# Kernel optimization log

Measured on AMD Instinct MI355X. Metric: run time of the kernel, lower is better.

Reference implementation:

```python
import jax, jax.numpy as jnp
import numpy as np

B, N, D = 16, 2048, 64

def setup_inputs() -> dict:
    key = jax.random.key(0)
    kq, kk, kv = jax.random.split(key, 3)
    q = jax.random.normal(kq, (B, N, D), dtype=jnp.float32)
    k = jax.random.normal(kk, (B, N, D), dtype=jnp.float32)
    v = jax.random.normal(kv, (B, N, D), dtype=jnp.float32)
    return {"q": q, "k": k, "v": v}

def reference(q, k, v):
    d_k = q.shape[-1]
    # scores: [B, N, N] = q @ k^T, scaled by 1/sqrt(d_k) (applied after matmul, as in source)
    scores = jnp.einsum('bnd,bmd->bnm', q, k)
    attn = jax.nn.softmax(scores / np.sqrt(d_k).astype(q.dtype), axis=-1)
    out = jnp.einsum('bnm,bmd->bnd', attn, v)
    return out
```

## Files before the change

kernel.cpp:

```cpp
#include <hip/hip_runtime.h>

#define B_  16
#define N_  2048
#define D_  64
#define QB  128
#define KB  64
#define NW  8

typedef __attribute__((ext_vector_type(8))) short short8;
typedef __attribute__((ext_vector_type(4))) float f32x4;

static __device__ __forceinline__ unsigned cvt_pk_bf16(float lo, float hi) {
  unsigned r;
  asm("v_cvt_pk_bf16_f32 %0, %1, %2" : "=v"(r) : "v"(lo), "v"(hi));
  return r;
}

union U8 { unsigned u[4]; short8 s8; };

__global__ __launch_bounds__(512, 2) void attn_fwd_kernel(
    const float* __restrict__ qg, const float* __restrict__ kg,
    const float* __restrict__ vg, float* __restrict__ outg) {
  __shared__ __align__(16) unsigned short Kl[KB * D_];
  __shared__ __align__(16) unsigned short Vt[D_ * KB];
  __shared__ __align__(16) unsigned short Pl[NW][16 * KB];

  const int tid = threadIdx.x;
  const int w  = tid >> 6;
  const int l  = tid & 63;
  const int g  = l >> 4;
  const int qi = l & 15;
  const int bidx = blockIdx.x;
  const int b  = bidx >> 4;
  const int qt = bidx & 15;
  const int q0 = qt * QB + w * 16;

  short8 qf[2];
  {
    const float* qp = qg + ((size_t)(b * N_ + q0 + qi)) * D_;
    const float s = 0.125f;
#pragma unroll
    for (int dc = 0; dc < 2; ++dc) {
      float4 f0 = *(const float4*)(qp + dc * 32 + g * 8);
      float4 f1 = *(const float4*)(qp + dc * 32 + g * 8 + 4);
      U8 u;
      u.u[0] = cvt_pk_bf16(f0.x * s, f0.y * s);
      u.u[1] = cvt_pk_bf16(f0.z * s, f0.w * s);
      u.u[2] = cvt_pk_bf16(f1.x * s, f1.y * s);
      u.u[3] = cvt_pk_bf16(f1.z * s, f1.w * s);
      qf[dc] = u.s8;
    }
  }

  f32x4 acc[4] = {{0,0,0,0},{0,0,0,0},{0,0,0,0},{0,0,0,0}};
  float m_run = -INFINITY;
  float l_run = 0.f;

  const float* kbase = kg + (size_t)b * N_ * D_;
  const float* vbase = vg + (size_t)b * N_ * D_;

  for (int kv0 = 0; kv0 < N_; kv0 += KB) {
#pragma unroll
    for (int p = 0; p < 2; ++p) {
      int idx = tid + p * 512;
      int row = idx >> 4, c4 = idx & 15;
      float4 f = *(const float4*)(kbase + (size_t)(kv0 + row) * D_ + c4 * 4);
      unsigned u0 = cvt_pk_bf16(f.x, f.y);
      unsigned u1 = cvt_pk_bf16(f.z, f.w);
      int o = (row * 64 + c4 * 4) ^ ((row & 7) << 3);
      *(uint2*)&Kl[o] = make_uint2(u0, u1);
    }
    {
      int rp = tid >> 4, c4 = tid & 15;
      int row2 = rp * 2;
      const float* vp = vbase + (size_t)(kv0 + row2) * D_ + c4 * 4;
      float4 a0 = *(const float4*)vp;
      float4 a1 = *(const float4*)(vp + D_);
      float lo[4] = {a0.x, a0.y, a0.z, a0.w};
      float hi[4] = {a1.x, a1.y, a1.z, a1.w};
#pragma unroll
      for (int i = 0; i < 4; ++i) {
        int d = c4 * 4 + i;
        unsigned u = cvt_pk_bf16(lo[i], hi[i]);
        int o = (d * 64 + row2) ^ ((d & 7) << 3);
        *(unsigned*)&Vt[o] = u;
      }
    }
    __syncthreads();

    f32x4 st[4];
#pragma unroll
    for (int kvt = 0; kvt < 4; ++kvt) {
      int kvr = kvt * 16 + qi;
      int base = kvr * 64;
      int sw = (kvr & 7) << 3;
      short8 kf0 = *(const short8*)&Kl[(base + g * 8) ^ sw];
      short8 kf1 = *(const short8*)&Kl[(base + 32 + g * 8) ^ sw];
      f32x4 z = {0, 0, 0, 0};
      z = __builtin_amdgcn_mfma_f32_16x16x32_bf16(kf0, qf[0], z, 0, 0, 0);
      z = __builtin_amdgcn_mfma_f32_16x16x32_bf16(kf1, qf[1], z, 0, 0, 0);
      st[kvt] = z;
    }

    float mloc = -INFINITY;
#pragma unroll
    for (int kvt = 0; kvt < 4; ++kvt)
#pragma unroll
      for (int r = 0; r < 4; ++r) mloc = fmaxf(mloc, st[kvt][r]);
    mloc = fmaxf(mloc, __shfl_xor(mloc, 16));
    mloc = fmaxf(mloc, __shfl_xor(mloc, 32));
    float mnew  = fmaxf(m_run, mloc);
    float alpha = __expf(m_run - mnew);
    m_run = mnew;

    float ps = 0.f;
#pragma unroll
    for (int kvt = 0; kvt < 4; ++kvt)
#pragma unroll
      for (int r = 0; r < 4; ++r) {
        float p = __expf(st[kvt][r] - mnew);
        st[kvt][r] = p;
        ps += p;
      }
    ps += __shfl_xor(ps, 16);
    ps += __shfl_xor(ps, 32);
    l_run = l_run * alpha + ps;

#pragma unroll
    for (int dt = 0; dt < 4; ++dt)
#pragma unroll
      for (int r = 0; r < 4; ++r) acc[dt][r] *= alpha;

#pragma unroll
    for (int kvt = 0; kvt < 4; ++kvt) {
      unsigned u0 = cvt_pk_bf16(st[kvt][0], st[kvt][1]);
      unsigned u1 = cvt_pk_bf16(st[kvt][2], st[kvt][3]);
      int kv = kvt * 16 + g * 4;
      int sw = (qi & 7) << 3;
      *(unsigned*)&Pl[w][(qi * 64 + kv) ^ sw]     = u0;
      *(unsigned*)&Pl[w][(qi * 64 + kv + 2) ^ sw] = u1;
    }
    asm volatile("s_waitcnt lgkmcnt(0)" ::: "memory");

#pragma unroll
    for (int kk = 0; kk < 2; ++kk) {
      short8 pf = *(const short8*)&Pl[w][(qi * 64 + kk * 32 + g * 8) ^ ((qi & 7) << 3)];
#pragma unroll
      for (int dt = 0; dt < 4; ++dt) {
        int d = dt * 16 + qi;
        short8 vf = *(const short8*)&Vt[(d * 64 + kk * 32 + g * 8) ^ ((d & 7) << 3)];
        acc[dt] = __builtin_amdgcn_mfma_f32_16x16x32_bf16(vf, pf, acc[dt], 0, 0, 0);
      }
    }
    __syncthreads();
  }

  float rl = 1.0f / l_run;
  float* op = outg + ((size_t)(b * N_ + q0 + qi)) * D_;
#pragma unroll
  for (int dt = 0; dt < 4; ++dt) {
    float4 o;
    o.x = acc[dt][0] * rl;
    o.y = acc[dt][1] * rl;
    o.z = acc[dt][2] * rl;
    o.w = acc[dt][3] * rl;
    *(float4*)(op + dt * 16 + g * 4) = o;
  }
}

extern "C" void kernel_launch(void* const* d_in, const int* in_sizes, int n_in,
                              void* d_out, int out_size, void* d_ws, size_t ws_size,
                              hipStream_t stream) {
  const float* q = (const float*)d_in[0];
  const float* k = (const float*)d_in[1];
  const float* v = (const float*)d_in[2];
  float* out = (float*)d_out;
  dim3 grid(B_ * (N_ / QB));
  dim3 block(512);
  attn_fwd_kernel<<<grid, block, 0, stream>>>(q, k, v, out);
}
```

Baseline: 121.7 us.

## Precompute bf16 K/V tile images and double-buffer them via direct global-to-LDS loads

Adds a prep kernel that converts K and V to bf16 once, already swizzled and with V transposed, and writes them to workspace. The main attention kernel then streams these tiles into double-buffered LDS with global_load_lds so the next tile loads while the current one computes. This removes the per-block fp32 loads and conversions that every query tile repeated. It also switches to exp2 with log2e folded into the Q scale, skips the rescale unless the running max grows by more than 8, raises wave priority around the MFMAs, and remaps block indices. The cost is an extra launch, a workspace round trip, and a fallback path when the workspace is too small.

```diff
diff --git a/kernel.cpp b/kernel.cpp
--- a/kernel.cpp
+++ b/kernel.cpp
@@ -5,40 +5,101 @@
 #define D_  64
 #define QB  128
 #define KB  64
+#define NT  (N_/KB)
 #define NW  8
+#define TILE_ELEMS (KB * D_)
 
 typedef __attribute__((ext_vector_type(8))) short short8;
 typedef __attribute__((ext_vector_type(4))) float f32x4;
+typedef unsigned short u16_t;
 
 static __device__ __forceinline__ unsigned cvt_pk_bf16(float lo, float hi) {
   unsigned r;
   asm("v_cvt_pk_bf16_f32 %0, %1, %2" : "=v"(r) : "v"(lo), "v"(hi));
   return r;
 }
+static __device__ __forceinline__ float exp2_fast(float x) {
+  float r;
+  asm("v_exp_f32 %0, %1" : "=v"(r) : "v"(x));
+  return r;
+}
+static __device__ __forceinline__ void gload_lds16(const void* g, void* l) {
+  __builtin_amdgcn_global_load_lds(
+      (const __attribute__((address_space(1))) unsigned*)g,
+      (__attribute__((address_space(3))) unsigned*)l, 16, 0, 0);
+}
 
 union U8 { unsigned u[4]; short8 s8; };
 
-__global__ __launch_bounds__(512, 2) void attn_fwd_kernel(
-    const float* __restrict__ qg, const float* __restrict__ kg,
-    const float* __restrict__ vg, float* __restrict__ outg) {
-  __shared__ __align__(16) unsigned short Kl[KB * D_];
-  __shared__ __align__(16) unsigned short Vt[D_ * KB];
-  __shared__ __align__(16) unsigned short Pl[NW][16 * KB];
-
+__global__ __launch_bounds__(256) void prep_kernel(
+    const float* __restrict__ kg, const float* __restrict__ vg,
+    u16_t* __restrict__ kimg, u16_t* __restrict__ vimg) {
+  const int bid = blockIdx.x;
+  const int isV = bid & 1;
+  const int tileid = bid >> 1;
+  const float* src = (isV ? vg : kg) + (size_t)tileid * TILE_ELEMS;
+  u16_t* dst = (isV ? vimg : kimg) + (size_t)tileid * TILE_ELEMS;
   const int tid = threadIdx.x;
-  const int w  = tid >> 6;
-  const int l  = tid & 63;
-  const int g  = l >> 4;
-  const int qi = l & 15;
+
+  if (!isV) {
+#pragma unroll
+    for (int p = 0; p < 2; ++p) {
+      int c = tid + p * 256;
+      int row = c >> 3, c8 = c & 7;
+      const float* sp = src + row * 64 + c8 * 8;
+      float4 f0 = *(const float4*)sp;
+      float4 f1 = *(const float4*)(sp + 4);
+      uint4 u;
+      u.x = cvt_pk_bf16(f0.x, f0.y);
+      u.y = cvt_pk_bf16(f0.z, f0.w);
+      u.z = cvt_pk_bf16(f1.x, f1.y);
+      u.w = cvt_pk_bf16(f1.z, f1.w);
+      *(uint4*)&dst[(row * 64 + c8 * 8) ^ ((row & 7) << 3)] = u;
+    }
+  } else {
+    __shared__ float Vl[64][68];
+    int row = tid >> 2, q4 = (tid & 3) * 16;
+    const float* sp = src + row * 64 + q4;
+#pragma unroll
+    for (int i = 0; i < 4; ++i)
+      *(float4*)&Vl[row][q4 + i * 4] = *(const float4*)(sp + i * 4);
+    __syncthreads();
+#pragma unroll
+    for (int p = 0; p < 2; ++p) {
+      int c = tid + p * 256;
+      int d = c >> 3, kc = c & 7;
+      float x[8];
+#pragma unroll
+      for (int j = 0; j < 8; ++j) x[j] = Vl[kc * 8 + j][d];
+      uint4 u;
+      u.x = cvt_pk_bf16(x[0], x[1]);
+      u.y = cvt_pk_bf16(x[2], x[3]);
+      u.z = cvt_pk_bf16(x[4], x[5]);
+      u.w = cvt_pk_bf16(x[6], x[7]);
+      *(uint4*)&dst[(d * 64 + kc * 8) ^ ((d & 7) << 3)] = u;
+    }
+  }
+}
+
+__global__ __launch_bounds__(512, 2) void attn_main(
+    const float* __restrict__ qg, const u16_t* __restrict__ kimg,
+    const u16_t* __restrict__ vimg, float* __restrict__ outg) {
+  __shared__ __align__(16) u16_t Kl[2][TILE_ELEMS];
+  __shared__ __align__(16) u16_t Vt[2][TILE_ELEMS];
+  __shared__ __align__(16) u16_t Pl[NW][16 * KB];
+
+  const int tid = threadIdx.x;
+  const int w = tid >> 6, l = tid & 63;
+  const int g = l >> 4, qi = l & 15;
   const int bidx = blockIdx.x;
-  const int b  = bidx >> 4;
-  const int qt = bidx & 15;
+  const int logical = (bidx & 7) * 32 + (bidx >> 3);
+  const int b = logical >> 4, qt = logical & 15;
   const int q0 = qt * QB + w * 16;
 
   short8 qf[2];
   {
+    const float s = 0.18033688011112042f;
     const float* qp = qg + ((size_t)(b * N_ + q0 + qi)) * D_;
-    const float s = 0.125f;
 #pragma unroll
     for (int dc = 0; dc < 2; ++dc) {
       float4 f0 = *(const float4*)(qp + dc * 32 + g * 8);
@@ -56,6 +117,142 @@
   float m_run = -INFINITY;
   float l_run = 0.f;
 
+  const u16_t* kt = kimg + (size_t)b * NT * TILE_ELEMS;
+  const u16_t* vt = vimg + (size_t)b * NT * TILE_ELEMS;
+
+  auto stage = [&](int bb, int tt) {
+    const u16_t* kp = kt + (size_t)tt * TILE_ELEMS + w * 512 + l * 8;
+    const u16_t* vp = vt + (size_t)tt * TILE_ELEMS + w * 512 + l * 8;
+    gload_lds16(kp, &Kl[bb][w * 512]);
+    gload_lds16(vp, &Vt[bb][w * 512]);
+  };
+
+  stage(0, 0);
+  __syncthreads();
+
+  for (int t = 0; t < NT; ++t) {
+    const int cur = t & 1;
+    if (t + 1 < NT) stage(cur ^ 1, t + 1);
+    const u16_t* Kc = Kl[cur];
+    const u16_t* Vc = Vt[cur];
+
+    f32x4 st[4];
+    __builtin_amdgcn_s_setprio(1);
+#pragma unroll
+    for (int kvt = 0; kvt < 4; ++kvt) {
+      int kvr = kvt * 16 + qi;
+      int base = kvr * 64, sw = (kvr & 7) << 3;
+      short8 kf0 = *(const short8*)&Kc[(base + g * 8) ^ sw];
+      short8 kf1 = *(const short8*)&Kc[(base + 32 + g * 8) ^ sw];
+      f32x4 z = {0, 0, 0, 0};
+      z = __builtin_amdgcn_mfma_f32_16x16x32_bf16(kf0, qf[0], z, 0, 0, 0);
+      z = __builtin_amdgcn_mfma_f32_16x16x32_bf16(kf1, qf[1], z, 0, 0, 0);
+      st[kvt] = z;
+    }
+    __builtin_amdgcn_s_setprio(0);
+
+    float m01 = fmaxf(fmaxf(st[0][0], st[0][1]), fmaxf(st[0][2], st[0][3]));
+    float m23 = fmaxf(fmaxf(st[1][0], st[1][1]), fmaxf(st[1][2], st[1][3]));
+    float m45 = fmaxf(fmaxf(st[2][0], st[2][1]), fmaxf(st[2][2], st[2][3]));
+    float m67 = fmaxf(fmaxf(st[3][0], st[3][1]), fmaxf(st[3][2], st[3][3]));
+    float mloc = fmaxf(fmaxf(m01, m23), fmaxf(m45, m67));
+    mloc = fmaxf(mloc, __shfl_xor(mloc, 16));
+    mloc = fmaxf(mloc, __shfl_xor(mloc, 32));
+    if (__any(mloc > m_run + 8.0f)) {
+      float mnew = fmaxf(m_run, mloc);
+      float alpha = exp2_fast(m_run - mnew);
+      m_run = mnew;
+      l_run *= alpha;
+#pragma unroll
+      for (int dt = 0; dt < 4; ++dt)
+#pragma unroll
+        for (int r = 0; r < 4; ++r) acc[dt][r] *= alpha;
+    }
+    float ps = 0.f;
+#pragma unroll
+    for (int kvt = 0; kvt < 4; ++kvt)
+#pragma unroll
+      for (int r = 0; r < 4; ++r) {
+        float p = exp2_fast(st[kvt][r] - m_run);
+        st[kvt][r] = p;
+        ps += p;
+      }
+    ps += __shfl_xor(ps, 16);
+    ps += __shfl_xor(ps, 32);
+    l_run += ps;
+
+#pragma unroll
+    for (int kvt = 0; kvt < 4; ++kvt) {
+      unsigned u0 = cvt_pk_bf16(st[kvt][0], st[kvt][1]);
+      unsigned u1 = cvt_pk_bf16(st[kvt][2], st[kvt][3]);
+      int kv = kvt * 16 + g * 4;
+      int sw = (qi & 7) << 3;
+      *(unsigned*)&Pl[w][(qi * 64 + kv) ^ sw]     = u0;
+      *(unsigned*)&Pl[w][(qi * 64 + kv + 2) ^ sw] = u1;
+    }
+    asm volatile("s_waitcnt lgkmcnt(0)" ::: "memory");
+
+    __builtin_amdgcn_s_setprio(1);
+#pragma unroll
+    for (int kk = 0; kk < 2; ++kk) {
+      short8 pf = *(const short8*)&Pl[w][(qi * 64 + kk * 32 + g * 8) ^ ((qi & 7) << 3)];
+#pragma unroll
+      for (int dt = 0; dt < 4; ++dt) {
+        int d = dt * 16 + qi;
+        short8 vf = *(const short8*)&Vc[(d * 64 + kk * 32 + g * 8) ^ ((d & 7) << 3)];
+        acc[dt] = __builtin_amdgcn_mfma_f32_16x16x32_bf16(vf, pf, acc[dt], 0, 0, 0);
+      }
+    }
+    __builtin_amdgcn_s_setprio(0);
+    __syncthreads();
+  }
+
+  float rl = 1.0f / l_run;
+  float* op = outg + ((size_t)(b * N_ + q0 + qi)) * D_;
+#pragma unroll
+  for (int dt = 0; dt < 4; ++dt) {
+    float4 o;
+    o.x = acc[dt][0] * rl;
+    o.y = acc[dt][1] * rl;
+    o.z = acc[dt][2] * rl;
+    o.w = acc[dt][3] * rl;
+    *(float4*)(op + dt * 16 + g * 4) = o;
+  }
+}
+
+__global__ __launch_bounds__(512, 2) void attn_fwd_fallback(
+    const float* __restrict__ qg, const float* __restrict__ kg,
+    const float* __restrict__ vg, float* __restrict__ outg) {
+  __shared__ __align__(16) u16_t Kl[KB * D_];
+  __shared__ __align__(16) u16_t Vt[D_ * KB];
+  __shared__ __align__(16) u16_t Pl[NW][16 * KB];
+
+  const int tid = threadIdx.x;
+  const int w = tid >> 6, l = tid & 63;
+  const int g = l >> 4, qi = l & 15;
+  const int bidx = blockIdx.x;
+  const int b = bidx >> 4, qt = bidx & 15;
+  const int q0 = qt * QB + w * 16;
+
+  short8 qf[2];
+  {
+    const float* qp = qg + ((size_t)(b * N_ + q0 + qi)) * D_;
+    const float s = 0.125f;
+#pragma unroll
+    for (int dc = 0; dc < 2; ++dc) {
+      float4 f0 = *(const float4*)(qp + dc * 32 + g * 8);
+      float4 f1 = *(const float4*)(qp + dc * 32 + g * 8 + 4);
+      U8 u;
+      u.u[0] = cvt_pk_bf16(f0.x * s, f0.y * s);
+      u.u[1] = cvt_pk_bf16(f0.z * s, f0.w * s);
+      u.u[2] = cvt_pk_bf16(f1.x * s, f1.y * s);
+      u.u[3] = cvt_pk_bf16(f1.z * s, f1.w * s);
+      qf[dc] = u.s8;
+    }
+  }
+
+  f32x4 acc[4] = {{0,0,0,0},{0,0,0,0},{0,0,0,0},{0,0,0,0}};
+  float m_run = -INFINITY, l_run = 0.f;
   const float* kbase = kg + (size_t)b * N_ * D_;
   const float* vbase = vg + (size_t)b * N_ * D_;
 
@@ -92,8 +289,7 @@
 #pragma unroll
     for (int kvt = 0; kvt < 4; ++kvt) {
       int kvr = kvt * 16 + qi;
-      int base = kvr * 64;
-      int sw = (kvr & 7) << 3;
+      int base = kvr * 64, sw = (kvr & 7) << 3;
       short8 kf0 = *(const short8*)&Kl[(base + g * 8) ^ sw];
       short8 kf1 = *(const short8*)&Kl[(base + 32 + g * 8) ^ sw];
       f32x4 z = {0, 0, 0, 0};
@@ -109,7 +305,7 @@
       for (int r = 0; r < 4; ++r) mloc = fmaxf(mloc, st[kvt][r]);
     mloc = fmaxf(mloc, __shfl_xor(mloc, 16));
     mloc = fmaxf(mloc, __shfl_xor(mloc, 32));
-    float mnew  = fmaxf(m_run, mloc);
+    float mnew = fmaxf(m_run, mloc);
     float alpha = __expf(m_run - mnew);
     m_run = mnew;
 
@@ -175,7 +371,16 @@
   const float* k = (const float*)d_in[1];
   const float* v = (const float*)d_in[2];
   float* out = (float*)d_out;
-  dim3 grid(B_ * (N_ / QB));
-  dim3 block(512);
-  attn_fwd_kernel<<<grid, block, 0, stream>>>(q, k, v, out);
-}
+
+  const size_t img_elems = (size_t)B_ * N_ * D_;
+  const size_t need = 2 * img_elems * sizeof(u16_t);
+
+  if (ws_size >= need) {
+    u16_t* kimg = (u16_t*)d_ws;
+    u16_t* vimg = kimg + img_elems;
+    prep_kernel<<<dim3(B_ * NT * 2), dim3(256), 0, stream>>>(k, v, kimg, vimg);
+    attn_main<<<dim3(B_ * (N_ / QB)), dim3(512), 0, stream>>>(q, kimg, vimg, out);
+  } else {
+    attn_fwd_fallback<<<dim3(B_ * (N_ / QB)), dim3(512), 0, stream>>>(q, k, v, out);
+  }
+}
```

Measured after the change: 117.8 us. -3.2%, faster.
